# Optimization experiments

Hardware: AMD Instinct MI355X
Metric: run time of the kernel (lower is better)

## Reference

```python
import jax, jax.numpy as jnp
import numpy as np

D_MODEL = 1024
N_HEADS = 16
D_K = D_MODEL // N_HEADS
D_FF = 4096
B, S = 2, 2048
LN_EPS = 1e-5
NEG_INF = -1e30  # finite stand-in for -inf; first (all-masked) row is overwritten by zeros anyway


def layer_norm(x, g, b):
    mu = jnp.mean(x, axis=-1, keepdims=True)
    var = jnp.mean(jnp.square(x - mu), axis=-1, keepdims=True)
    return (x - mu) * jax.lax.rsqrt(var + LN_EPS) * g + b


def setup_inputs() -> dict:
    key = jax.random.key(0)
    ks = jax.random.split(key, 16)
    sd = 0.02
    inp = {
        "query": jax.random.normal(ks[0], (B, S, D_MODEL), jnp.float32),
        "key": jax.random.normal(ks[1], (B, S, D_MODEL), jnp.float32),
        "values": jax.random.normal(ks[2], (B, S, D_MODEL), jnp.float32),
        "Wq": jax.random.normal(ks[3], (D_MODEL, D_MODEL), jnp.float32) * sd,
        "bq": jnp.zeros((D_MODEL,), jnp.float32),
        "Wk": jax.random.normal(ks[4], (D_MODEL, D_MODEL), jnp.float32) * sd,
        "bk": jnp.zeros((D_MODEL,), jnp.float32),
        "Wv": jax.random.normal(ks[5], (D_MODEL, D_MODEL), jnp.float32) * sd,
        "bv": jnp.zeros((D_MODEL,), jnp.float32),
        "Wo": jax.random.normal(ks[6], (D_MODEL, D_MODEL), jnp.float32) * sd,
        "bo": jnp.zeros((D_MODEL,), jnp.float32),
        "ln1_g": jnp.ones((D_MODEL,), jnp.float32),
        "ln1_b": jnp.zeros((D_MODEL,), jnp.float32),
        "W1": jax.random.normal(ks[7], (D_MODEL, D_FF), jnp.float32) * sd,
        "b1": jnp.zeros((D_FF,), jnp.float32),
        "W2": jax.random.normal(ks[8], (D_FF, D_MODEL), jnp.float32) * sd,
        "b2": jnp.zeros((D_MODEL,), jnp.float32),
        "ln2_g": jnp.ones((D_MODEL,), jnp.float32),
        "ln2_b": jnp.zeros((D_MODEL,), jnp.float32),
        "mask": 0,
    }
    return inp


def reference(query, key, values, Wq, bq, Wk, bk, Wv, bv, Wo, bo,
              ln1_g, ln1_b, W1, b1, W2, b2, ln2_g, ln2_b, mask):
    b, s, d = query.shape
    # projections -> [B, H, S, d_k]
    q = (query @ Wq + bq).reshape(b, s, N_HEADS, D_K).transpose(0, 2, 1, 3)
    k = (key @ Wk + bk).reshape(b, s, N_HEADS, D_K).transpose(0, 2, 1, 3)
    v = (values @ Wv + bv).reshape(b, s, N_HEADS, D_K).transpose(0, 2, 1, 3)
    # scores [B, H, S, S]
    scores = jnp.einsum("bhqd,bhkd->bhqk", q, k) / jnp.sqrt(jnp.float32(D_K))
    # torch: triu(ones, k=mask)==0 -> allowed iff j < i + mask
    i = jnp.arange(s)[:, None]
    j = jnp.arange(s)[None, :]
    allowed = j < (i + mask)
    scores = jnp.where(allowed, scores, NEG_INF)
    attn = jax.nn.softmax(scores, axis=-1)
    if mask == 0:
        # zero-pad trick: first query row (fully masked) is replaced by zeros
        attn = attn.at[:, :, 0, :].set(0.0)
    ctx = jnp.einsum("bhqk,bhkd->bhqd", attn, v)
    ctx = ctx.transpose(0, 2, 1, 3).reshape(b, s, d)
    attn_out = ctx @ Wo + bo
    x = layer_norm(query + attn_out, ln1_g, ln1_b)
    ffn = jax.nn.relu(x @ W1 + b1) @ W2 + b2
    out = layer_norm(x + ffn, ln2_g, ln2_b)
    return out
```

## Files before the change

### kernel.cpp

```cpp
#include <hip/hip_runtime.h>


typedef __attribute__((ext_vector_type(8))) __bf16 bf16x8;
typedef __attribute__((ext_vector_type(4))) float f32x4;

struct alignas(8)  S4 { short x, y, z, w; };
struct alignas(16) F4 { float x, y, z, w; };
struct alignas(16) I4 { int x, y, z, w; };

static __device__ __forceinline__ short f2bf(float f) {
  unsigned u = __float_as_uint(f);
  u += 0x7fff + ((u >> 16) & 1);
  return (short)(u >> 16);
}

static __device__ __forceinline__ void store_out(float* p, float v) { *p = v; }
static __device__ __forceinline__ void store_out(short* p, float v) { *p = f2bf(v); }

#define GLL16(g, l)                                                         \
  __builtin_amdgcn_global_load_lds(                                         \
      (__attribute__((address_space(1))) void*)(g),                         \
      (__attribute__((address_space(3))) void*)(l), 16, 0, 0)

__global__ __launch_bounds__(256) void cvt_bf16_kernel(
    const float* __restrict__ i0, const float* __restrict__ i1,
    const float* __restrict__ i2, short* __restrict__ o0,
    short* __restrict__ o1, short* __restrict__ o2) {
  int z = blockIdx.y;
  const float* in = z == 0 ? i0 : (z == 1 ? i1 : i2);
  short* out = z == 0 ? o0 : (z == 1 ? o1 : o2);
  int i = (blockIdx.x * 256 + threadIdx.x) * 4;
  F4 v = *(const F4*)(in + i);
  S4 o = { f2bf(v.x), f2bf(v.y), f2bf(v.z), f2bf(v.w) };
  *(S4*)(out + i) = o;
}

__global__ __launch_bounds__(256) void transpose_cvt_kernel(
    const float* __restrict__ Wq, const float* __restrict__ Wk,
    const float* __restrict__ Wv, const float* __restrict__ Wo,
    const float* __restrict__ W1, const float* __restrict__ W2,
    short* __restrict__ Wqt, short* __restrict__ Wkt,
    short* __restrict__ Wvt, short* __restrict__ Wot,
    short* __restrict__ W1t, short* __restrict__ W2t) {
  __shared__ float tile[64][65];
  int bid = blockIdx.x;
  const float* W; short* Wt; int K, N, kx, ny;
  if (bid < 1024) {
    int w = bid >> 8, t = bid & 255;
    W = w == 0 ? Wq : (w == 1 ? Wk : (w == 2 ? Wv : Wo));
    Wt = w == 0 ? Wqt : (w == 1 ? Wkt : (w == 2 ? Wvt : Wot));
    K = 1024; N = 1024; kx = t & 15; ny = t >> 4;
  } else if (bid < 2048) {
    int t = bid - 1024;
    W = W1; Wt = W1t; K = 1024; N = 4096; kx = t & 15; ny = t >> 4;
  } else {
    int t = bid - 2048;
    W = W2; Wt = W2t; K = 4096; N = 1024; kx = t & 63; ny = t >> 6;
  }
  int k0 = kx * 64, n0 = ny * 64;
  int tid = threadIdx.x;
  int rr = tid >> 4, cc = (tid & 15) * 4;
#pragma unroll
  for (int p = 0; p < 4; ++p) {
    int row = p * 16 + rr;
    F4 v = *(const F4*)&W[(long)(k0 + row) * N + n0 + cc];
    tile[row][cc] = v.x; tile[row][cc + 1] = v.y;
    tile[row][cc + 2] = v.z; tile[row][cc + 3] = v.w;
  }
  __syncthreads();
#pragma unroll
  for (int p = 0; p < 4; ++p) {
    int rn = p * 16 + rr;
    S4 o = { f2bf(tile[cc + 0][rn]), f2bf(tile[cc + 1][rn]),
             f2bf(tile[cc + 2][rn]), f2bf(tile[cc + 3][rn]) };
    *(S4*)&Wt[(long)(n0 + rn) * K + k0 + cc] = o;
  }
}

template <int OUT_MODE, bool RELU, bool RES, typename OT>
__device__ __forceinline__ void gemm_core(
    const short* __restrict__ A, const short* __restrict__ Bt,
    const float* __restrict__ bias, const float* __restrict__ res,
    OT* __restrict__ out, int M, int N, int K, int kBeg, int kEnd) {
  __shared__ __align__(16) short sA[128 * 64];
  __shared__ __align__(16) short sB[128 * 64];
  int tid = threadIdx.x;
  int lane = tid & 63, wave = tid >> 6;
  int col = lane & 15, quad = lane >> 4;
  int m0 = blockIdx.x * 128, n0 = blockIdx.y * 128;
  int wm = (wave & 1) * 64, wn = (wave >> 1) * 64;

  f32x4 acc[4][4] = {};

  for (int k0 = kBeg; k0 < kEnd; k0 += 64) {
    __syncthreads();
#pragma unroll
    for (int j = 0; j < 4; ++j) {
      int idx = j * 256 + tid;
      int row = idx >> 3, cp = idx & 7;
      int c = cp ^ (row & 7);
      const short* ga = A  + (long)(m0 + row) * K + k0 + c * 8;
      const short* gb = Bt + (long)(n0 + row) * K + k0 + c * 8;
      short* la = &sA[(j * 256 + (wave << 6)) * 8];
      short* lb = &sB[(j * 256 + (wave << 6)) * 8];
      GLL16(ga, la);
      GLL16(gb, lb);
    }
    __syncthreads();

#pragma unroll
    for (int kk = 0; kk < 2; ++kk) {
      bf16x8 a[4], b[4];
#pragma unroll
      for (int t = 0; t < 4; ++t) {
        int ra = wm + t * 16 + col;
        int ca = kk * 4 + quad;
        a[t] = *(const bf16x8*)&sA[ra * 64 + ((ca ^ (ra & 7)) << 3)];
        int rb = wn + t * 16 + col;
        b[t] = *(const bf16x8*)&sB[rb * 64 + ((ca ^ (rb & 7)) << 3)];
      }
#pragma unroll
      for (int t = 0; t < 4; ++t)
#pragma unroll
        for (int u = 0; u < 4; ++u)
          acc[t][u] = __builtin_amdgcn_mfma_f32_16x16x32_bf16(
              a[t], b[u], acc[t][u], 0, 0, 0);
    }
  }

#pragma unroll
  for (int t = 0; t < 4; ++t) {
#pragma unroll
    for (int u = 0; u < 4; ++u) {
      int Cc = n0 + wn + u * 16 + col;
      float bv = bias ? bias[Cc] : 0.f;
#pragma unroll
      for (int r = 0; r < 4; ++r) {
        int R = m0 + wm + t * 16 + quad * 4 + r;
        float v = acc[t][u][r] + bv;
        if (RES) v += res[(long)R * N + Cc];
        if (RELU) v = v > 0.f ? v : 0.f;
        if (OUT_MODE == 0) {
          store_out(&out[(long)R * N + Cc], v);
        } else {
          int bb = R >> 11, s = R & 2047, h = Cc >> 6, d = Cc & 63;
          store_out(&out[((long)((bb * 16 + h) * 2048 + s) << 6) + d], v);
        }
      }
    }
  }
}

template <int OUT_MODE, bool RELU, bool RES, typename OT>
__global__ __launch_bounds__(256) void gemm_bt(
    const short* __restrict__ A, const short* __restrict__ Bt,
    const float* __restrict__ bias, const float* __restrict__ res,
    OT* __restrict__ out, int M, int N, int K) {
  gemm_core<OUT_MODE, RELU, RES, OT>(A, Bt, bias, res, out, M, N, K, 0, K);
}

__global__ __launch_bounds__(256) void gemm_splitk(
    const short* __restrict__ A, const short* __restrict__ Bt,
    const float* __restrict__ bias, float* __restrict__ p0,
    float* __restrict__ p1, int M, int N, int K) {
  int z = blockIdx.z;
  float* out = z == 0 ? p0 : p1;
  const float* b = z == 0 ? bias : nullptr;
  int kc = K >> 1;
  gemm_core<0, false, false, float>(A, Bt, b, nullptr, out, M, N, K,
                                    z * kc, z * kc + kc);
}

__global__ __launch_bounds__(256) void gemm_qkv(
    const short* __restrict__ Aq, const short* __restrict__ Ak,
    const short* __restrict__ Av, const short* __restrict__ Btq,
    const short* __restrict__ Btk, const short* __restrict__ Btv,
    const float* __restrict__ bq, const float* __restrict__ bk,
    const float* __restrict__ bv, short* __restrict__ Qp,
    short* __restrict__ Kp, short* __restrict__ Vp) {
  int z = blockIdx.z;
  const short* A = z == 0 ? Aq : (z == 1 ? Ak : Av);
  const short* Bt = z == 0 ? Btq : (z == 1 ? Btk : Btv);
  const float* bias = z == 0 ? bq : (z == 1 ? bk : bv);
  short* out = z == 0 ? Qp : (z == 1 ? Kp : Vp);
  gemm_core<1, false, false, short>(A, Bt, bias, nullptr, out,
                                    4096, 1024, 1024, 0, 1024);
}

__global__ __launch_bounds__(512) void attn_kernel(
    const short* __restrict__ Q, const short* __restrict__ K,
    const short* __restrict__ V, const int* __restrict__ maskp,
    short* __restrict__ ctx) {
  __shared__ __align__(16) short sK[2][64 * 64];
  __shared__ __align__(16) int   sVt[2][64 * 32];
  __shared__ __align__(16) short sP[8 * 16 * 64];
  int tid = threadIdx.x, wave = tid >> 6;
  int lane = tid & 63;
  int col = lane & 15, quad = lane >> 4;
  int bh = blockIdx.x, pair = blockIdx.y;
  int maskv = maskp[0];
  const long base = (long)bh * (2048 * 64);
  int b = bh >> 4, h = bh & 15;

  int kp = tid & 31, dg = tid >> 5, d0v = dg * 4;

  for (int pass = 0; pass < 2; ++pass) {
    int qt = pass ? (15 - pair) : pair;
    int i0 = qt * 128 + wave * 16;

    long jmax = (long)qt * 128 + 127 + maskv - 1;
    int tot = (jmax < 0) ? 0 : (int)(jmax >> 6) + 1;
    if (tot > 32) tot = 32;

    bf16x8 aQ[2];
#pragma unroll
    for (int kk = 0; kk < 2; ++kk)
      aQ[kk] = *(const bf16x8*)&Q[base + (long)(i0 + col) * 64 + kk * 32 + quad * 8];

    f32x4 o[4] = {};
    float lsum[4] = { 0.f, 0.f, 0.f, 0.f };

    if (tot > 0) {
      {
        int row = tid >> 3, cp = tid & 7;
        int c = cp ^ (row & 7);
        GLL16(K + base + (long)row * 64 + c * 8,
              &sK[0][(wave << 6) * 8]);
      }
      {
        union { S4 v; short s[4]; } u0, u1;
        u0.v = *(const S4*)&V[base + (long)(2 * kp) * 64 + d0v];
        u1.v = *(const S4*)&V[base + (long)(2 * kp + 1) * 64 + d0v];
#pragma unroll
        for (int j = 0; j < 4; ++j) {
          int d = d0v + j;
          int w = ((int)(unsigned short)u1.s[j] << 16) | (unsigned short)u0.s[j];
          sVt[0][d * 32 + ((((kp >> 2) ^ (d & 7)) << 2) | (kp & 3))] = w;
        }
      }
    }
    __syncthreads();

    for (int kt = 0; kt < tot; ++kt) {
      int cur = kt & 1, nxt = cur ^ 1;
      bool pf = (kt + 1 < tot);

      union { S4 v; short s[4]; } u0, u1;
      if (pf) {
        int row = tid >> 3, cp = tid & 7;
        int c = cp ^ (row & 7);
        GLL16(K + base + (long)((kt + 1) * 64 + row) * 64 + c * 8,
              &sK[nxt][(wave << 6) * 8]);
        u0.v = *(const S4*)&V[base + (long)((kt + 1) * 64 + 2 * kp) * 64 + d0v];
        u1.v = *(const S4*)&V[base + (long)((kt + 1) * 64 + 2 * kp + 1) * 64 + d0v];
      }

      f32x4 sc[4] = {};
#pragma unroll
      for (int kk = 0; kk < 2; ++kk) {
        int ca = kk * 4 + quad;
#pragma unroll
        for (int nt = 0; nt < 4; ++nt) {
          int rk = nt * 16 + col;
          bf16x8 bK = *(const bf16x8*)&sK[cur][rk * 64 + ((ca ^ (rk & 7)) << 3)];
          sc[nt] = __builtin_amdgcn_mfma_f32_16x16x32_bf16(aQ[kk], bK, sc[nt], 0, 0, 0);
        }
      }

      bool interior = (kt * 64 + 63) < (i0 + maskv);
      if (interior) {
#pragma unroll
        for (int r = 0; r < 4; ++r) {
          int qr = quad * 4 + r;
#pragma unroll
          for (int nt = 0; nt < 4; ++nt) {
            float p = __expf(sc[nt][r] * 0.125f);
            lsum[r] += p;
            int k8 = nt * 2 + (col >> 3);
            sP[wave * 1024 + qr * 64 + (((k8 ^ (qr & 7)) << 3) | (col & 7))] =
                f2bf(p);
          }
        }
      } else {
#pragma unroll
        for (int r = 0; r < 4; ++r) {
          int i = i0 + quad * 4 + r;
          int qr = quad * 4 + r;
#pragma unroll
          for (int nt = 0; nt < 4; ++nt) {
            int j = kt * 64 + nt * 16 + col;
            float p = (j < i + maskv) ? __expf(sc[nt][r] * 0.125f) : 0.f;
            lsum[r] += p;
            int k8 = nt * 2 + (col >> 3);
            sP[wave * 1024 + qr * 64 + (((k8 ^ (qr & 7)) << 3) | (col & 7))] =
                f2bf(p);
          }
        }
      }

#pragma unroll
      for (int kk = 0; kk < 2; ++kk) {
        int ca = kk * 4 + quad;
        bf16x8 aP = *(const bf16x8*)&sP[wave * 1024 + col * 64 + ((ca ^ (col & 7)) << 3)];
#pragma unroll
        for (int dt = 0; dt < 4; ++dt) {
          int d = dt * 16 + col;
          bf16x8 bV = *(const bf16x8*)((const short*)sVt[cur] + d * 64 + ((ca ^ (d & 7)) << 3));
          o[dt] = __builtin_amdgcn_mfma_f32_16x16x32_bf16(aP, bV, o[dt], 0, 0, 0);
        }
      }

      if (pf) {
#pragma unroll
        for (int j = 0; j < 4; ++j) {
          int d = d0v + j;
          int w = ((int)(unsigned short)u1.s[j] << 16) | (unsigned short)u0.s[j];
          sVt[nxt][d * 32 + ((((kp >> 2) ^ (d & 7)) << 2) | (kp & 3))] = w;
        }
      }
      __syncthreads();
    }

#pragma unroll
    for (int r = 0; r < 4; ++r)
#pragma unroll
      for (int off = 1; off < 16; off <<= 1)
        lsum[r] += __shfl_xor(lsum[r], off);

#pragma unroll
    for (int r = 0; r < 4; ++r) {
      int i = i0 + quad * 4 + r;
      float inv = (lsum[r] > 0.f) ? 1.f / lsum[r] : 0.f;
      if (maskv == 0 && i == 0) inv = 0.f;
#pragma unroll
      for (int dt = 0; dt < 4; ++dt)
        ctx[(long)(b * 2048 + i) * 1024 + h * 64 + dt * 16 + col] =
            f2bf(o[dt][r] * inv);
    }
    __syncthreads();
  }
}

__global__ __launch_bounds__(256) void ln_comb_kernel(
    const float* __restrict__ p0, const float* __restrict__ p1,
    const float* __restrict__ res, const float* __restrict__ g,
    const float* __restrict__ b, float* __restrict__ outf,
    short* __restrict__ outb) {
  int r = blockIdx.x, tid = threadIdx.x;
  int lane = tid & 63, wave = tid >> 6;
  long off0 = (long)r * 1024;
  F4 a = ((const F4*)(p0 + off0))[tid];
  F4 c = ((const F4*)(p1 + off0))[tid];
  F4 d = ((const F4*)(res + off0))[tid];
  F4 v = { a.x + c.x + d.x, a.y + c.y + d.y, a.z + c.z + d.z, a.w + c.w + d.w };
  float s = v.x + v.y + v.z + v.w;
  float sq = v.x * v.x + v.y * v.y + v.z * v.z + v.w * v.w;
#pragma unroll
  for (int off = 1; off < 64; off <<= 1) {
    s += __shfl_xor(s, off);
    sq += __shfl_xor(sq, off);
  }
  __shared__ float rs[4], rq[4];
  if (lane == 0) { rs[wave] = s; rq[wave] = sq; }
  __syncthreads();
  s = rs[0] + rs[1] + rs[2] + rs[3];
  sq = rq[0] + rq[1] + rq[2] + rq[3];
  float mu = s * (1.0f / 1024.0f);
  float var = sq * (1.0f / 1024.0f) - mu * mu;
  float rstd = rsqrtf(var + 1e-5f);
  F4 gv = ((const F4*)g)[tid], bv = ((const F4*)b)[tid];
  F4 o;
  o.x = (v.x - mu) * rstd * gv.x + bv.x;
  o.y = (v.y - mu) * rstd * gv.y + bv.y;
  o.z = (v.z - mu) * rstd * gv.z + bv.z;
  o.w = (v.w - mu) * rstd * gv.w + bv.w;
  ((F4*)(outf + off0))[tid] = o;
  if (outb) {
    S4 ob = { f2bf(o.x), f2bf(o.y), f2bf(o.z), f2bf(o.w) };
    ((S4*)(outb + off0))[tid] = ob;
  }
}

extern "C" void kernel_launch(void* const* d_in, const int* in_sizes, int n_in,
                              void* d_out, int out_size, void* d_ws, size_t ws_size,
                              hipStream_t stream) {
  const float* query  = (const float*)d_in[0];
  const float* keyi   = (const float*)d_in[1];
  const float* values = (const float*)d_in[2];
  const float* Wq = (const float*)d_in[3];
  const float* bq = (const float*)d_in[4];
  const float* Wk = (const float*)d_in[5];
  const float* bk = (const float*)d_in[6];
  const float* Wv = (const float*)d_in[7];
  const float* bv = (const float*)d_in[8];
  const float* Wo = (const float*)d_in[9];
  const float* bo = (const float*)d_in[10];
  const float* ln1_g = (const float*)d_in[11];
  const float* ln1_b = (const float*)d_in[12];
  const float* W1 = (const float*)d_in[13];
  const float* b1 = (const float*)d_in[14];
  const float* W2 = (const float*)d_in[15];
  const float* b2 = (const float*)d_in[16];
  const float* ln2_g = (const float*)d_in[17];
  const float* ln2_b = (const float*)d_in[18];
  const int*   maskp = (const int*)d_in[19];
  float* out = (float*)d_out;

  char* ws = (char*)d_ws;
  const size_t MB = 1u << 20;
  short* q_bf = (short*)(ws + 0);
  short* k_bf = (short*)(ws + 8 * MB);
  short* v_bf = (short*)(ws + 16 * MB);
  short* ctx  = (short*)(ws + 24 * MB);
  short* Qp   = (short*)(ws + 32 * MB);
  short* Kp   = (short*)(ws + 40 * MB);
  short* Vp   = (short*)(ws + 48 * MB);
  short* Wqt  = (short*)(ws + 56 * MB);
  short* Wkt  = (short*)(ws + 58 * MB);
  short* Wvt  = (short*)(ws + 60 * MB);
  short* Wot  = (short*)(ws + 62 * MB);
  short* W1t  = (short*)(ws + 64 * MB);
  short* W2t  = (short*)(ws + 72 * MB);
  short* hbuf = (short*)(ws + 80 * MB);
  float* pWo0 = (float*)(ws + 0);
  float* pWo1 = (float*)(ws + 32 * MB);
  float* x_f32 = (float*)(ws + 16 * MB);
  short* x_bf  = (short*)(ws + 48 * MB);
  float* pF0 = (float*)(ws + 0);
  float* pF1 = (float*)(ws + 32 * MB);

  cvt_bf16_kernel<<<dim3(4096, 3), 256, 0, stream>>>(query, keyi, values,
                                                     q_bf, k_bf, v_bf);
  transpose_cvt_kernel<<<3072, 256, 0, stream>>>(Wq, Wk, Wv, Wo, W1, W2,
                                                 Wqt, Wkt, Wvt, Wot, W1t, W2t);
  gemm_qkv<<<dim3(32, 8, 3), 256, 0, stream>>>(q_bf, k_bf, v_bf,
                                               Wqt, Wkt, Wvt,
                                               bq, bk, bv, Qp, Kp, Vp);
  attn_kernel<<<dim3(32, 8), 512, 0, stream>>>(Qp, Kp, Vp, maskp, ctx);
  gemm_splitk<<<dim3(32, 8, 2), 256, 0, stream>>>(ctx, Wot, bo, pWo0, pWo1,
                                                  4096, 1024, 1024);
  ln_comb_kernel<<<4096, 256, 0, stream>>>(pWo0, pWo1, query, ln1_g, ln1_b,
                                           x_f32, x_bf);
  gemm_bt<0, true, false, short><<<dim3(32, 32), 256, 0, stream>>>(
      x_bf, W1t, b1, nullptr, hbuf, 4096, 4096, 1024);
  gemm_splitk<<<dim3(32, 8, 2), 256, 0, stream>>>(hbuf, W2t, b2, pF0, pF1,
                                                  4096, 1024, 4096);
  ln_comb_kernel<<<4096, 256, 0, stream>>>(pF0, pF1, x_f32, ln2_g, ln2_b,
                                           out, nullptr);

  (void)in_sizes; (void)n_in; (void)out_size; (void)ws_size;
}
```

Measured before the change: 408.9 us.

## Split attention into 64-row query tiles, one per block, heaviest first

The attention kernel used 512-thread blocks that each processed two paired 128-row query tiles (light plus heavy) to balance causal work. It now launches 1024 blocks of 256 threads, each handling a single 64-row query tile, with tiles scheduled in descending order of work so the heaviest start first. K/V staging loads are widened to 8 elements per thread to fit the smaller block. This aims for more blocks and better load balance across CUs, at the cost of K/V tiles being reloaded by more blocks.

```diff
diff --git a/kernel.cpp b/kernel.cpp
--- a/kernel.cpp
+++ b/kernel.cpp
@@ -3,6 +3,7 @@
 
 typedef __attribute__((ext_vector_type(8))) __bf16 bf16x8;
 typedef __attribute__((ext_vector_type(4))) float f32x4;
+typedef __attribute__((ext_vector_type(8))) short s16x8;
 
 struct alignas(8)  S4 { short x, y, z, w; };
 struct alignas(16) F4 { float x, y, z, w; };
@@ -187,157 +188,159 @@
                                     4096, 1024, 1024, 0, 1024);
 }
 
-__global__ __launch_bounds__(512) void attn_kernel(
+__global__ __launch_bounds__(256) void attn_kernel(
     const short* __restrict__ Q, const short* __restrict__ K,
     const short* __restrict__ V, const int* __restrict__ maskp,
     short* __restrict__ ctx) {
   __shared__ __align__(16) short sK[2][64 * 64];
   __shared__ __align__(16) int   sVt[2][64 * 32];
-  __shared__ __align__(16) short sP[8 * 16 * 64];
+  __shared__ __align__(16) short sP[4 * 16 * 64];
   int tid = threadIdx.x, wave = tid >> 6;
   int lane = tid & 63;
   int col = lane & 15, quad = lane >> 4;
-  int bh = blockIdx.x, pair = blockIdx.y;
+  int bh = blockIdx.x;
+  int qt = 31 - blockIdx.y;
   int maskv = maskp[0];
   const long base = (long)bh * (2048 * 64);
   int b = bh >> 4, h = bh & 15;
 
-  int kp = tid & 31, dg = tid >> 5, d0v = dg * 4;
-
-  for (int pass = 0; pass < 2; ++pass) {
-    int qt = pass ? (15 - pair) : pair;
-    int i0 = qt * 128 + wave * 16;
-
-    long jmax = (long)qt * 128 + 127 + maskv - 1;
-    int tot = (jmax < 0) ? 0 : (int)(jmax >> 6) + 1;
-    if (tot > 32) tot = 32;
-
-    bf16x8 aQ[2];
-#pragma unroll
-    for (int kk = 0; kk < 2; ++kk)
-      aQ[kk] = *(const bf16x8*)&Q[base + (long)(i0 + col) * 64 + kk * 32 + quad * 8];
-
-    f32x4 o[4] = {};
-    float lsum[4] = { 0.f, 0.f, 0.f, 0.f };
-
-    if (tot > 0) {
-      {
-        int row = tid >> 3, cp = tid & 7;
-        int c = cp ^ (row & 7);
-        GLL16(K + base + (long)row * 64 + c * 8,
-              &sK[0][(wave << 6) * 8]);
-      }
-      {
-        union { S4 v; short s[4]; } u0, u1;
-        u0.v = *(const S4*)&V[base + (long)(2 * kp) * 64 + d0v];
-        u1.v = *(const S4*)&V[base + (long)(2 * kp + 1) * 64 + d0v];
-#pragma unroll
-        for (int j = 0; j < 4; ++j) {
-          int d = d0v + j;
-          int w = ((int)(unsigned short)u1.s[j] << 16) | (unsigned short)u0.s[j];
-          sVt[0][d * 32 + ((((kp >> 2) ^ (d & 7)) << 2) | (kp & 3))] = w;
-        }
-      }
-    }
-    __syncthreads();
-
-    for (int kt = 0; kt < tot; ++kt) {
-      int cur = kt & 1, nxt = cur ^ 1;
-      bool pf = (kt + 1 < tot);
-
-      union { S4 v; short s[4]; } u0, u1;
-      if (pf) {
-        int row = tid >> 3, cp = tid & 7;
+  int kp = tid & 31, dg = tid >> 5, d0v = dg * 8;
+
+  int i0 = qt * 64 + wave * 16;
+
+  long jmax = (long)qt * 64 + 63 + maskv - 1;
+  int tot = (jmax < 0) ? 0 : (int)(jmax >> 6) + 1;
+  if (tot > 32) tot = 32;
+
+  bf16x8 aQ[2];
+#pragma unroll
+  for (int kk = 0; kk < 2; ++kk)
+    aQ[kk] = *(const bf16x8*)&Q[base + (long)(i0 + col) * 64 + kk * 32 + quad * 8];
+
+  f32x4 o[4] = {};
+  float lsum[4] = { 0.f, 0.f, 0.f, 0.f };
+
+  if (tot > 0) {
+#pragma unroll
+    for (int j = 0; j < 2; ++j) {
+      int idx = j * 256 + tid;
+      int row = idx >> 3, cp = idx & 7;
+      int c = cp ^ (row & 7);
+      GLL16(K + base + (long)row * 64 + c * 8,
+            &sK[0][(j * 256 + (wave << 6)) * 8]);
+    }
+    {
+      s16x8 u0 = *(const s16x8*)&V[base + (long)(2 * kp) * 64 + d0v];
+      s16x8 u1 = *(const s16x8*)&V[base + (long)(2 * kp + 1) * 64 + d0v];
+#pragma unroll
+      for (int j = 0; j < 8; ++j) {
+        int d = d0v + j;
+        int w = ((int)(unsigned short)u1[j] << 16) | (unsigned short)u0[j];
+        sVt[0][d * 32 + ((((kp >> 2) ^ (d & 7)) << 2) | (kp & 3))] = w;
+      }
+    }
+  }
+  __syncthreads();
+
+  for (int kt = 0; kt < tot; ++kt) {
+    int cur = kt & 1, nxt = cur ^ 1;
+    bool pf = (kt + 1 < tot);
+
+    s16x8 u0, u1;
+    if (pf) {
+#pragma unroll
+      for (int j = 0; j < 2; ++j) {
+        int idx = j * 256 + tid;
+        int row = idx >> 3, cp = idx & 7;
         int c = cp ^ (row & 7);
         GLL16(K + base + (long)((kt + 1) * 64 + row) * 64 + c * 8,
-              &sK[nxt][(wave << 6) * 8]);
-        u0.v = *(const S4*)&V[base + (long)((kt + 1) * 64 + 2 * kp) * 64 + d0v];
-        u1.v = *(const S4*)&V[base + (long)((kt + 1) * 64 + 2 * kp + 1) * 64 + d0v];
-      }
-
-      f32x4 sc[4] = {};
-#pragma unroll
-      for (int kk = 0; kk < 2; ++kk) {
-        int ca = kk * 4 + quad;
+              &sK[nxt][(j * 256 + (wave << 6)) * 8]);
+      }
+      u0 = *(const s16x8*)&V[base + (long)((kt + 1) * 64 + 2 * kp) * 64 + d0v];
+      u1 = *(const s16x8*)&V[base + (long)((kt + 1) * 64 + 2 * kp + 1) * 64 + d0v];
+    }
+
+    f32x4 sc[4] = {};
+#pragma unroll
+    for (int kk = 0; kk < 2; ++kk) {
+      int ca = kk * 4 + quad;
+#pragma unroll
+      for (int nt = 0; nt < 4; ++nt) {
+        int rk = nt * 16 + col;
+        bf16x8 bK = *(const bf16x8*)&sK[cur][rk * 64 + ((ca ^ (rk & 7)) << 3)];
+        sc[nt] = __builtin_amdgcn_mfma_f32_16x16x32_bf16(aQ[kk], bK, sc[nt], 0, 0, 0);
+      }
+    }
+
+    bool interior = (kt * 64 + 63) < (i0 + maskv);
+    if (interior) {
+#pragma unroll
+      for (int r = 0; r < 4; ++r) {
+        int qr = quad * 4 + r;
 #pragma unroll
         for (int nt = 0; nt < 4; ++nt) {
-          int rk = nt * 16 + col;
-          bf16x8 bK = *(const bf16x8*)&sK[cur][rk * 64 + ((ca ^ (rk & 7)) << 3)];
-          sc[nt] = __builtin_amdgcn_mfma_f32_16x16x32_bf16(aQ[kk], bK, sc[nt], 0, 0, 0);
+          float p = __expf(sc[nt][r] * 0.125f);
+          lsum[r] += p;
+          int k8 = nt * 2 + (col >> 3);
+          sP[wave * 1024 + qr * 64 + (((k8 ^ (qr & 7)) << 3) | (col & 7))] =
+              f2bf(p);
         }
       }
-
-      bool interior = (kt * 64 + 63) < (i0 + maskv);
-      if (interior) {
-#pragma unroll
-        for (int r = 0; r < 4; ++r) {
-          int qr = quad * 4 + r;
-#pragma unroll
-          for (int nt = 0; nt < 4; ++nt) {
-            float p = __expf(sc[nt][r] * 0.125f);
-            lsum[r] += p;
-            int k8 = nt * 2 + (col >> 3);
-            sP[wave * 1024 + qr * 64 + (((k8 ^ (qr & 7)) << 3) | (col & 7))] =
-                f2bf(p);
-          }
+    } else {
+#pragma unroll
+      for (int r = 0; r < 4; ++r) {
+        int i = i0 + quad * 4 + r;
+        int qr = quad * 4 + r;
+#pragma unroll
+        for (int nt = 0; nt < 4; ++nt) {
+          int j = kt * 64 + nt * 16 + col;
+          float p = (j < i + maskv) ? __expf(sc[nt][r] * 0.125f) : 0.f;
+          lsum[r] += p;
+          int k8 = nt * 2 + (col >> 3);
+          sP[wave * 1024 + qr * 64 + (((k8 ^ (qr & 7)) << 3) | (col & 7))] =
+              f2bf(p);
         }
-      } else {
-#pragma unroll
-        for (int r = 0; r < 4; ++r) {
-          int i = i0 + quad * 4 + r;
-          int qr = quad * 4 + r;
-#pragma unroll
-          for (int nt = 0; nt < 4; ++nt) {
-            int j = kt * 64 + nt * 16 + col;
-            float p = (j < i + maskv) ? __expf(sc[nt][r] * 0.125f) : 0.f;
-            lsum[r] += p;
-            int k8 = nt * 2 + (col >> 3);
-            sP[wave * 1024 + qr * 64 + (((k8 ^ (qr & 7)) << 3) | (col & 7))] =
-                f2bf(p);
-          }
-        }
-      }
-
-#pragma unroll
-      for (int kk = 0; kk < 2; ++kk) {
-        int ca = kk * 4 + quad;
-        bf16x8 aP = *(const bf16x8*)&sP[wave * 1024 + col * 64 + ((ca ^ (col & 7)) << 3)];
-#pragma unroll
-        for (int dt = 0; dt < 4; ++dt) {
-          int d = dt * 16 + col;
-          bf16x8 bV = *(const bf16x8*)((const short*)sVt[cur] + d * 64 + ((ca ^ (d & 7)) << 3));
-          o[dt] = __builtin_amdgcn_mfma_f32_16x16x32_bf16(aP, bV, o[dt], 0, 0, 0);
-        }
-      }
-
-      if (pf) {
-#pragma unroll
-        for (int j = 0; j < 4; ++j) {
-          int d = d0v + j;
-          int w = ((int)(unsigned short)u1.s[j] << 16) | (unsigned short)u0.s[j];
-          sVt[nxt][d * 32 + ((((kp >> 2) ^ (d & 7)) << 2) | (kp & 3))] = w;
-        }
-      }
-      __syncthreads();
-    }
-
-#pragma unroll
-    for (int r = 0; r < 4; ++r)
-#pragma unroll
-      for (int off = 1; off < 16; off <<= 1)
-        lsum[r] += __shfl_xor(lsum[r], off);
-
-#pragma unroll
-    for (int r = 0; r < 4; ++r) {
-      int i = i0 + quad * 4 + r;
-      float inv = (lsum[r] > 0.f) ? 1.f / lsum[r] : 0.f;
-      if (maskv == 0 && i == 0) inv = 0.f;
-#pragma unroll
-      for (int dt = 0; dt < 4; ++dt)
-        ctx[(long)(b * 2048 + i) * 1024 + h * 64 + dt * 16 + col] =
-            f2bf(o[dt][r] * inv);
+      }
+    }
+
+#pragma unroll
+    for (int kk = 0; kk < 2; ++kk) {
+      int ca = kk * 4 + quad;
+      bf16x8 aP = *(const bf16x8*)&sP[wave * 1024 + col * 64 + ((ca ^ (col & 7)) << 3)];
+#pragma unroll
+      for (int dt = 0; dt < 4; ++dt) {
+        int d = dt * 16 + col;
+        bf16x8 bV = *(const bf16x8*)((const short*)sVt[cur] + d * 64 + ((ca ^ (d & 7)) << 3));
+        o[dt] = __builtin_amdgcn_mfma_f32_16x16x32_bf16(aP, bV, o[dt], 0, 0, 0);
+      }
+    }
+
+    if (pf) {
+#pragma unroll
+      for (int j = 0; j < 8; ++j) {
+        int d = d0v + j;
+        int w = ((int)(unsigned short)u1[j] << 16) | (unsigned short)u0[j];
+        sVt[nxt][d * 32 + ((((kp >> 2) ^ (d & 7)) << 2) | (kp & 3))] = w;
+      }
     }
     __syncthreads();
+  }
+
+#pragma unroll
+  for (int r = 0; r < 4; ++r)
+#pragma unroll
+    for (int off = 1; off < 16; off <<= 1)
+      lsum[r] += __shfl_xor(lsum[r], off);
+
+#pragma unroll
+  for (int r = 0; r < 4; ++r) {
+    int i = i0 + quad * 4 + r;
+    float inv = (lsum[r] > 0.f) ? 1.f / lsum[r] : 0.f;
+    if (maskv == 0 && i == 0) inv = 0.f;
+#pragma unroll
+    for (int dt = 0; dt < 4; ++dt)
+      ctx[(long)(b * 2048 + i) * 1024 + h * 64 + dt * 16 + col] =
+          f2bf(o[dt][r] * inv);
   }
 }
 
@@ -436,7 +439,7 @@
   gemm_qkv<<<dim3(32, 8, 3), 256, 0, stream>>>(q_bf, k_bf, v_bf,
                                                Wqt, Wkt, Wvt,
                                                bq, bk, bv, Qp, Kp, Vp);
-  attn_kernel<<<dim3(32, 8), 512, 0, stream>>>(Qp, Kp, Vp, maskp, ctx);
+  attn_kernel<<<dim3(32, 32), 256, 0, stream>>>(Qp, Kp, Vp, maskp, ctx);
   gemm_splitk<<<dim3(32, 8, 2), 256, 0, stream>>>(ctx, Wot, bo, pWo0, pWo1,
                                                   4096, 1024, 1024);
   ln_comb_kernel<<<4096, 256, 0, stream>>>(pWo0, pWo1, query, ln1_g, ln1_b,
```

After: 397.9 us. -2.7%, faster.
